# Optimization experiments

Hardware: AMD Instinct MI355X
Metric: run time of the kernel (lower is better)

The kernel has to match this reference:

```python
import jax, jax.numpy as jnp
import numpy as np

B, S, D, H, M = 4, 2048, 1024, 16, 128
DH = D // H
SCALE = jnp.float32(np.sqrt(D / H))


def setup_inputs() -> dict:
    key = jax.random.key(0)
    ks = jax.random.split(key, 4)
    x = jax.random.normal(ks[0], (B, S, D), dtype=jnp.float32)
    mask = jnp.zeros((B, 1, 1, S), dtype=bool)
    W_in = jax.random.normal(ks[1], (3 * D, D), dtype=jnp.float32) * 0.02
    b_in = jnp.zeros((3 * D,), dtype=jnp.float32)
    pos_emb = jax.random.normal(ks[2], (2 * M + 1, DH), dtype=jnp.float32)
    W_out = jax.random.normal(ks[3], (D, D), dtype=jnp.float32) * 0.02
    b_out = jnp.zeros((D,), dtype=jnp.float32)
    return {"x": x, "mask": mask, "W_in": W_in, "b_in": b_in,
            "pos_emb": pos_emb, "W_out": W_out, "b_out": b_out}


def _arrange_pos(pos_emb, seq_len, max_len):
    k = jnp.arange(seq_len)
    q = jnp.arange(seq_len)
    idx = jnp.clip(k[None, :] - q[:, None], -max_len, max_len) + max_len  # [S,S]
    return pos_emb[idx]  # [S,S,DH]


def reference(x, mask, W_in, b_in, pos_emb, W_out, b_out):
    b, s, d = x.shape
    qkv = x @ W_in.T + b_in                      # [B,S,3D]
    qkv = qkv.reshape(b, s, H, 3 * DH).transpose(0, 2, 1, 3)  # [B,H,S,3DH]
    Q, K, V = jnp.split(qkv, 3, axis=3)          # each [B,H,S,DH]
    logits = jnp.einsum('bhqd,bhkd->bhqk', Q, K)
    rel = _arrange_pos(pos_emb, s, M)            # [S,S,DH] (q,k,dh)
    pos_logits = jnp.einsum('bhqd,qkd->bhqk', Q, rel)
    logits = (logits + pos_logits) / SCALE
    logits = jnp.where(mask, -jnp.inf, logits)
    attn = jax.nn.softmax(logits, axis=3)
    combined = jnp.einsum('bhqk,bhkd->bhqd', attn, V)
    out = combined.transpose(0, 2, 1, 3).reshape(b, s, d)  # concat heads
    return out @ W_out.T + b_out
```

## Files before the change

### kernel.cpp

```cpp
#include <hip/hip_runtime.h>
#include <hip/hip_bf16.h>
#include <math.h>

#define SS 2048
#define HH 16
#define NPOS 257
#define C_SCALE 0.18033688f
#define P_THR 256.0f

typedef short  s16x8 __attribute__((ext_vector_type(8)));
typedef float  f32x4 __attribute__((ext_vector_type(4)));
typedef unsigned u32x4 __attribute__((ext_vector_type(4)));

__device__ __forceinline__ unsigned short f2bf(float f) {
    unsigned u = __builtin_bit_cast(unsigned, f);
    u += 0x7fff + ((u >> 16) & 1);
    return (unsigned short)(u >> 16);
}
__device__ __forceinline__ float bf2f(unsigned short b) {
    return __builtin_bit_cast(float, (unsigned)b << 16);
}
__device__ __forceinline__ s16x8 pack8(float4 a, float4 b) {
    s16x8 v;
    v[0]=(short)f2bf(a.x); v[1]=(short)f2bf(a.y); v[2]=(short)f2bf(a.z); v[3]=(short)f2bf(a.w);
    v[4]=(short)f2bf(b.x); v[5]=(short)f2bf(b.y); v[6]=(short)f2bf(b.z); v[7]=(short)f2bf(b.w);
    return v;
}
__device__ __forceinline__ unsigned cvtpk(float lo, float hi) {
    unsigned r;
    asm("v_cvt_pk_bf16_f32 %0, %1, %2" : "=v"(r) : "v"(lo), "v"(hi));
    return r;
}
__device__ __forceinline__ float exp2_fast(float x) {
    float r;
    asm("v_exp_f32 %0, %1" : "=v"(r) : "v"(x));
    return r;
}
__device__ __forceinline__ f32x4 mfma16(s16x8 a, s16x8 b, f32x4 c) {
    return __builtin_amdgcn_mfma_f32_16x16x32_bf16(a, b, c, 0, 0, 0);
}
__device__ __forceinline__ void gload_lds16(const void* gsrc, void* ldst) {
    __builtin_amdgcn_global_load_lds(
        (const __attribute__((address_space(1))) unsigned int*)gsrc,
        (__attribute__((address_space(3))) unsigned int*)ldst,
        16, 0, 0);
}
__device__ __forceinline__ int colp(int k) {
    return ((k >> 5) << 6) | (((k >> 2) & 3) << 4) | (((k >> 4) & 1) << 3) | ((k & 3) << 1);
}

__global__ __launch_bounds__(256)
void cvt_bf16(const float* __restrict__ in, unsigned short* __restrict__ out, int n8)
{
    for (int i = blockIdx.x * blockDim.x + threadIdx.x; i < n8; i += gridDim.x * blockDim.x) {
        const float4* p = (const float4*)(in + (size_t)i * 8);
        *(s16x8*)(out + (size_t)i * 8) = pack8(p[0], p[1]);
    }
}

__global__ __launch_bounds__(256)
void gemm_bf16_nt(const unsigned short* __restrict__ A,
                  const unsigned short* __restrict__ Bm,
                  const float* __restrict__ bias, float* __restrict__ Cout,
                  int Ndim, int Kdim)
{
    __shared__ short As[128 * 32];
    __shared__ short Bs[128 * 32];
    const int tid  = threadIdx.x;
    const int lane = tid & 63;
    const int wv   = tid >> 6;
    const int g    = lane >> 4;
    const int ln   = lane & 15;
    const int wm   = wv >> 1, wn = wv & 1;
    const int tm   = blockIdx.y << 7, tn = blockIdx.x << 7;
    const int srow  = lane >> 2;
    const int sslot = lane & 3;

    f32x4 acc[4][4];
#pragma unroll
    for (int mi = 0; mi < 4; ++mi)
#pragma unroll
        for (int ni = 0; ni < 4; ++ni) acc[mi][ni] = f32x4{0.f, 0.f, 0.f, 0.f};

    const unsigned short* Ab = A  + (size_t)(tm + wv*32 + srow) * Kdim + sslot*8;
    const unsigned short* Bb = Bm + (size_t)(tn + wv*32 + srow) * Kdim + sslot*8;
    const size_t rstep16 = (size_t)16 * Kdim;
    char* lA = (char*)As + (wv*32) * 64;
    char* lB = (char*)Bs + (wv*32) * 64;

    for (int k0 = 0; k0 < Kdim; k0 += 32) {
        __syncthreads();
        gload_lds16(Ab + k0,           lA);
        gload_lds16(Ab + k0 + rstep16, lA + 1024);
        gload_lds16(Bb + k0,           lB);
        gload_lds16(Bb + k0 + rstep16, lB + 1024);
        __syncthreads();

        s16x8 af[4], bf_[4];
#pragma unroll
        for (int mi = 0; mi < 4; ++mi)
            af[mi] = *(const s16x8*)((char*)As + (wm*64 + mi*16 + ln)*64 + g*16);
#pragma unroll
        for (int ni = 0; ni < 4; ++ni)
            bf_[ni] = *(const s16x8*)((char*)Bs + (wn*64 + ni*16 + ln)*64 + g*16);
#pragma unroll
        for (int mi = 0; mi < 4; ++mi)
#pragma unroll
            for (int ni = 0; ni < 4; ++ni)
                acc[mi][ni] = mfma16(af[mi], bf_[ni], acc[mi][ni]);
    }

#pragma unroll
    for (int ni = 0; ni < 4; ++ni) {
        const int col = tn + wn*64 + ni*16 + ln;
        const float bcol = bias[col];
#pragma unroll
        for (int mi = 0; mi < 4; ++mi)
#pragma unroll
            for (int j = 0; j < 4; ++j) {
                const int row = tm + wm*64 + mi*16 + 4*g + j;
                Cout[(size_t)row * Ndim + col] = acc[mi][ni][j] + bcol;
            }
    }
}

__global__ __launch_bounds__(256)
void gemm_qkv(const unsigned short* __restrict__ A,
              const unsigned short* __restrict__ Bm,
              const float* __restrict__ bias,
              unsigned short* __restrict__ qb,
              char* __restrict__ kbuf, char* __restrict__ vbuf)
{
    __shared__ short As[128 * 32];
    __shared__ short Bs[128 * 32];
    const int tid  = threadIdx.x;
    const int lane = tid & 63;
    const int wv   = tid >> 6;
    const int g    = lane >> 4;
    const int ln   = lane & 15;
    const int wm   = wv >> 1, wn = wv & 1;
    const int tm   = blockIdx.y << 7, tn = blockIdx.x << 7;
    const int srow  = lane >> 2;
    const int sslot = lane & 3;
    const int Kdim = 1024;

    f32x4 acc[4][4];
#pragma unroll
    for (int mi = 0; mi < 4; ++mi)
#pragma unroll
        for (int ni = 0; ni < 4; ++ni) acc[mi][ni] = f32x4{0.f, 0.f, 0.f, 0.f};

    const unsigned short* Ab = A  + (size_t)(tm + wv*32 + srow) * Kdim + sslot*8;
    const unsigned short* Bb = Bm + (size_t)(tn + wv*32 + srow) * Kdim + sslot*8;
    const size_t rstep16 = (size_t)16 * Kdim;
    char* lA = (char*)As + (wv*32) * 64;
    char* lB = (char*)Bs + (wv*32) * 64;

    for (int k0 = 0; k0 < Kdim; k0 += 32) {
        __syncthreads();
        gload_lds16(Ab + k0,           lA);
        gload_lds16(Ab + k0 + rstep16, lA + 1024);
        gload_lds16(Bb + k0,           lB);
        gload_lds16(Bb + k0 + rstep16, lB + 1024);
        __syncthreads();

        s16x8 af[4], bf_[4];
#pragma unroll
        for (int mi = 0; mi < 4; ++mi)
            af[mi] = *(const s16x8*)((char*)As + (wm*64 + mi*16 + ln)*64 + g*16);
#pragma unroll
        for (int ni = 0; ni < 4; ++ni)
            bf_[ni] = *(const s16x8*)((char*)Bs + (wn*64 + ni*16 + ln)*64 + g*16);
#pragma unroll
        for (int mi = 0; mi < 4; ++mi)
#pragma unroll
            for (int ni = 0; ni < 4; ++ni)
                acc[mi][ni] = mfma16(af[mi], bf_[ni], acc[mi][ni]);
    }

#pragma unroll
    for (int ni = 0; ni < 4; ++ni) {
        const int col  = tn + wn*64 + ni*16 + ln;
        const int col0 = tn + wn*64 + ni*16;
        const int h    = col0 / 192;
        const int r0   = col0 - h*192;
        const int r    = r0 + ln;
        const float bcol = bias[col];
#pragma unroll
        for (int mi = 0; mi < 4; ++mi) {
            const int rowb = tm + wm*64 + mi*16 + 4*g;
            const int bb = rowb >> 11, sl = rowb & 2047;
            const int kt = sl >> 6, kr = sl & 63;
            const size_t tile = ((size_t)(bb*HH + h)*32 + kt) * 8192;
            if (r0 < 64) {
                unsigned short* qp = qb + (((size_t)(bb*HH + h))*SS + sl)*64 + r;
#pragma unroll
                for (int j = 0; j < 4; ++j)
                    qp[(size_t)j*64] = f2bf((acc[mi][ni][j] + bcol) * C_SCALE);
            } else if (r0 < 128) {
                const int d = r - 64;
#pragma unroll
                for (int j = 0; j < 4; ++j) {
                    const int krj = kr + j;
                    *(unsigned short*)(kbuf + tile + krj*128 + ((2*d) ^ ((krj&7)<<4))) =
                        f2bf(acc[mi][ni][j] + bcol);
                }
            } else {
                const int d = r - 128;
                uint2 w;
                w.x = cvtpk(acc[mi][ni][0] + bcol, acc[mi][ni][1] + bcol);
                w.y = cvtpk(acc[mi][ni][2] + bcol, acc[mi][ni][3] + bcol);
                *(uint2*)(vbuf + tile + d*128 + (colp(kr) ^ ((d&7)<<4))) = w;
            }
        }
    }
}

#define FAR_LDS  32768
#define NEAR_LDS (16384 + 64*260*2)

__global__ __launch_bounds__(256, 4)
void attn_far(const unsigned short* __restrict__ qb,
              const char* __restrict__ kbuf, const char* __restrict__ vbuf,
              const unsigned short* __restrict__ pos_bf,
              float* __restrict__ o_state,
              float* __restrict__ m_state,
              float* __restrict__ l_state)
{
    extern __shared__ char smem[];
    char* ksb = smem;
    char* vtb = smem + 16384;

    const int tid = threadIdx.x, lane = tid & 63, wv = tid >> 6;
    const int g = lane >> 4, ln = lane & 15;
    const int fid = ((blockIdx.x & 7) << 7) | (blockIdx.x >> 3);
    const int q0 = (fid & 15) << 7, h = (fid >> 4) & 15, b = fid >> 8;
    const int q0w = q0 + wv*32;
    const int swz = (ln & 7) << 4;

    const unsigned short* qhb = qb + ((size_t)(b*HH + h))*SS*64;
    const char* ktile = kbuf + (size_t)(b*HH + h)*32*8192;
    const char* vtile = vbuf + (size_t)(b*HH + h)*32*8192;

    s16x8 qf[2][2];
#pragma unroll
    for (int gg = 0; gg < 2; ++gg) {
        const unsigned short* qp = qhb + (size_t)(q0w + 16*gg + ln) * 64;
        qf[gg][0] = *(const s16x8*)(qp + 8*g);
        qf[gg][1] = *(const s16x8*)(qp + 32 + 8*g);
    }

    const int ktA = max(0, (q0 - 128) >> 6);
    const int ktB = min(32, (q0 + 256) >> 6);
    const int gap = ktB - ktA, nfar = 32 - gap;

    char* kd0 = ksb + wv*2048;         char* kd1 = kd0 + 8192;
    char* vd0 = vtb + wv*2048;         char* vd1 = vd0 + 8192;
    const char* kbse0 = ksb + ln*128 + ((g*16) ^ swz);
    const char* kbse1 = ksb + ln*128 + ((64 + g*16) ^ swz);
    const char* vbse0 = vtb + ln*128 + ((g*16) ^ swz);
    const char* vbse1 = vtb + ln*128 + ((64 + g*16) ^ swz);

    const int sq0 = (ktA > 0) ? 0 : gap;
    const int sq1 = (1 < ktA) ? 1 : 1 + gap;
    const int sq2 = (2 < ktA) ? 2 : 2 + gap;

    {
        const char* s0k = ktile + (size_t)sq0*8192 + wv*2048 + lane*16;
        const char* s0v = vtile + (size_t)sq0*8192 + wv*2048 + lane*16;
        gload_lds16(s0k, kd0); gload_lds16(s0k + 1024, kd0 + 1024);
        gload_lds16(s0v, vd0); gload_lds16(s0v + 1024, vd0 + 1024);
        const char* s1k = ktile + (size_t)sq1*8192 + wv*2048 + lane*16;
        const char* s1v = vtile + (size_t)sq1*8192 + wv*2048 + lane*16;
        gload_lds16(s1k, kd1); gload_lds16(s1k + 1024, kd1 + 1024);
        gload_lds16(s1v, vd1); gload_lds16(s1v + 1024, vd1 + 1024);
    }
    const char* ksrc = ktile + (size_t)sq2*8192 + wv*2048 + lane*16;
    const char* vsrc = vtile + (size_t)sq2*8192 + wv*2048 + lane*16;

    float blo[2], bhi[2];
    {
        const int bsrc = (ln >> 2) << 4;
        const int s3 = ln & 3;
#pragma unroll
        for (int pass = 0; pass < 2; ++pass) {
            const int c  = pass*256 + ln;
            const int cc = c > 256 ? 256 : c;
            const unsigned short* pp = pos_bf + (size_t)cc * 64;
            s16x8 b0 = *(const s16x8*)(pp + 8*g);
            s16x8 b1 = *(const s16x8*)(pp + 32 + 8*g);
#pragma unroll
            for (int gg = 0; gg < 2; ++gg) {
                f32x4 d = {0,0,0,0};
                d = mfma16(qf[gg][0], b0, d);
                d = mfma16(qf[gg][1], b1, d);
                const float r0 = __shfl(d[0], bsrc, 64);
                const float r1 = __shfl(d[1], bsrc, 64);
                const float r2 = __shfl(d[2], bsrc, 64);
                const float r3 = __shfl(d[3], bsrc, 64);
                const float r = s3 == 0 ? r0 : s3 == 1 ? r1 : s3 == 2 ? r2 : r3;
                if (pass == 0) blo[gg] = r; else bhi[gg] = r;
            }
        }
    }

    f32x4 o[2][4], l[2];
    float m[2];
#pragma unroll
    for (int gg = 0; gg < 2; ++gg) {
        m[gg] = -INFINITY; l[gg] = f32x4{0,0,0,0};
#pragma unroll
        for (int dt = 0; dt < 4; ++dt) o[gg][dt] = f32x4{0,0,0,0};
    }
    s16x8 ONES;
#pragma unroll
    for (int i = 0; i < 8; ++i) ONES[i] = (short)0x3F80;

    asm volatile("s_waitcnt vmcnt(4)" ::: "memory");
    __builtin_amdgcn_sched_barrier(0);
    __builtin_amdgcn_s_barrier();
    __builtin_amdgcn_sched_barrier(0);

#define F_TILE(CUR, vv) do {                                                  \
                                  \
    f32x4 s[2][4];                                                            \
    _Pragma("unroll")                                                         \
    for (int gi = 0; gi < 2; ++gi)                                            \
        _Pragma("unroll")                                                     \
        for (int t = 0; t < 4; ++t) s[gi][t] = f32x4{0,0,0,0};                \
    __builtin_amdgcn_s_setprio(1);                                            \
    _Pragma("unroll")                                                         \
    for (int kc = 0; kc < 2; ++kc) {                                          \
        const char* kbx_ = (kc ? kbse1 : kbse0) + (CUR)*8192;                 \
        s16x8 kf[4];                                                          \
        _Pragma("unroll")                                                     \
        for (int t = 0; t < 4; ++t)                                           \
            kf[t] = *(const s16x8*)(kbx_ + t*2048);                           \
        _Pragma("unroll")                                                     \
        for (int t = 0; t < 4; ++t)                                           \
            _Pragma("unroll")                                                 \
            for (int gi = 0; gi < 2; ++gi)                                    \
                s[gi][t] = mfma16(kf[t], qf[gi][kc], s[gi][t]);               \
    }                                                                         \
    __builtin_amdgcn_s_setprio(0);                                            \
    const bool left_ = (vv) < ktA;                                            \
    u32x4 pa[2][2];                                                           \
    float pmax[2];                                                            \
    _Pragma("unroll")                                                         \
    for (int gi = 0; gi < 2; ++gi) {                                          \
        const float bmv = (left_ ? blo[gi] : bhi[gi]) - m[gi];                \
        float pm = 0.f;                                                       \
        _Pragma("unroll")                                                     \
        for (int t = 0; t < 4; ++t) {                                         \
            const float p0 = exp2_fast(s[gi][t][0] + bmv);                    \
            const float p1 = exp2_fast(s[gi][t][1] + bmv);                    \
            const float p2 = exp2_fast(s[gi][t][2] + bmv);                    \
            const float p3 = exp2_fast(s[gi][t][3] + bmv);                    \
            pm = fmaxf(pm, fmaxf(fmaxf(p0, p1), fmaxf(p2, p3)));              \
            pa[gi][t>>1][2*(t&1)]   = cvtpk(p0, p1);                          \
            pa[gi][t>>1][2*(t&1)+1] = cvtpk(p2, p3);                          \
        }                                                                     \
        pmax[gi] = pm;                                                        \
    }                                                                         \
    if (__any(fmaxf(pmax[0], pmax[1]) > P_THR)) {           \
        _Pragma("unroll")                                                     \
        for (int gi = 0; gi < 2; ++gi) {                                      \
            const float bc = left_ ? blo[gi] : bhi[gi];                       \
            float mr = s[gi][0][0];                                           \
            _Pragma("unroll")                                                 \
            for (int t = 0; t < 4; ++t)                                       \
                _Pragma("unroll")                                             \
                for (int j = 0; j < 4; ++j) mr = fmaxf(mr, s[gi][t][j]);      \
            mr = fmaxf(mr, __shfl_xor(mr, 16, 64));                           \
            mr = fmaxf(mr, __shfl_xor(mr, 32, 64));                           \
            const float nm = fmaxf(m[gi], mr + bc);                           \
            const float corr = exp2_fast(m[gi] - nm);                         \
            m[gi] = nm;                                                       \
            _Pragma("unroll")                                                 \
            for (int j = 0; j < 4; ++j) {                                     \
                const float cj = __shfl(corr, (lane & 48) + 4*g + j, 64);     \
                _Pragma("unroll")                                             \
                for (int dt = 0; dt < 4; ++dt) o[gi][dt][j] *= cj;            \
                l[gi][j] *= cj;                                               \
            }                                                                 \
            const float nb = bc - nm;                                         \
            _Pragma("unroll")                                                 \
            for (int t = 0; t < 4; ++t) {                                     \
                const float p0 = exp2_fast(s[gi][t][0] + nb);                 \
                const float p1 = exp2_fast(s[gi][t][1] + nb);                 \
                const float p2 = exp2_fast(s[gi][t][2] + nb);                 \
                const float p3 = exp2_fast(s[gi][t][3] + nb);                 \
                pa[gi][t>>1][2*(t&1)]   = cvtpk(p0, p1);                      \
                pa[gi][t>>1][2*(t&1)+1] = cvtpk(p2, p3);                      \
            }                                                                 \
        }                                                                     \
    }                                                                         \
    __builtin_amdgcn_s_setprio(1);                                            \
    _Pragma("unroll")                                                         \
    for (int kc = 0; kc < 2; ++kc) {                                          \
        const char* vbx_ = (kc ? vbse1 : vbse0) + (CUR)*8192;                 \
        _Pragma("unroll")                                                     \
        for (int dt = 0; dt < 4; ++dt) {                                      \
            const s16x8 bv = *(const s16x8*)(vbx_ + dt*2048);                 \
            _Pragma("unroll")                                                 \
            for (int gi = 0; gi < 2; ++gi)                                    \
                o[gi][dt] = mfma16(__builtin_bit_cast(s16x8, pa[gi][kc]), bv, o[gi][dt]); \
        }                                                                     \
        _Pragma("unroll")                                                     \
        for (int gi = 0; gi < 2; ++gi)                                        \
            l[gi] = mfma16(__builtin_bit_cast(s16x8, pa[gi][kc]), ONES, l[gi]); \
    }                                                                         \
    __builtin_amdgcn_s_setprio(0);                                            \
                                     \
    __builtin_amdgcn_s_barrier();                                             \
    __builtin_amdgcn_sched_barrier(0);                                        \
                                \
    if ((vv) + 2 < nfar) {                                                    \
        char* dk_ = (CUR) ? kd1 : kd0;                                        \
        char* dv_ = (CUR) ? vd1 : vd0;                                        \
        gload_lds16(ksrc, dk_); gload_lds16(ksrc + 1024, dk_ + 1024);         \
        gload_lds16(vsrc, dv_); gload_lds16(vsrc + 1024, dv_ + 1024);         \
        const int stp_ = (((vv) + 3) == ktA) ? (gap + 1) * 8192 : 8192;       \
        ksrc += stp_; vsrc += stp_;                                           \
    }                                                                         \
     \
    if ((vv) + 1 < nfar) {                                                    \
        if ((vv) + 2 < nfar) { asm volatile("s_waitcnt vmcnt(4)" ::: "memory"); } \
        else                 { asm volatile("s_waitcnt vmcnt(0)" ::: "memory"); } \
        __builtin_amdgcn_sched_barrier(0);                                    \
        __builtin_amdgcn_s_barrier();                                         \
        __builtin_amdgcn_sched_barrier(0);                                    \
    }                                                                         \
} while (0)

    for (int v = 0; v < nfar; v += 2) {
        F_TILE(0, v);
        F_TILE(1, v + 1);
    }

    const size_t rbase = (((size_t)(b*HH + h)) << 11) + q0w;
#pragma unroll
    for (int gg = 0; gg < 2; ++gg) {
        if (lane < 16) m_state[rbase + 16*gg + ln] = m[gg];
        if (ln == 0) {
#pragma unroll
            for (int j = 0; j < 4; ++j) l_state[rbase + 16*gg + 4*g + j] = l[gg][j];
        }
#pragma unroll
        for (int dt = 0; dt < 4; ++dt)
#pragma unroll
            for (int j = 0; j < 4; ++j)
                o_state[(rbase + 16*gg + 4*g + j)*64 + dt*16 + ln] = o[gg][dt][j];
    }
}

__global__ __launch_bounds__(256, 3)
void attn_near(const unsigned short* __restrict__ qb,
               const char* __restrict__ kbuf, const char* __restrict__ vbuf,
               const unsigned short* __restrict__ pos_bf,
               const float* __restrict__ o_state,
               const float* __restrict__ m_state,
               const float* __restrict__ l_state,
               unsigned short* __restrict__ comb)
{
    extern __shared__ char smem[];
    char* ksb = smem;
    unsigned short* tab = (unsigned short*)(smem + 16384);

    const int tid = threadIdx.x, lane = tid & 63, wv = tid >> 6;
    const int g = lane >> 4, ln = lane & 15;
    const int fid = ((blockIdx.x & 7) << 8) | (blockIdx.x >> 3);
    const int q0 = (fid & 31) << 6, h = (fid >> 5) & 15, b = fid >> 9;
    const int q0w = q0 + wv*16;
    const int swz = (ln & 7) << 4;

    const unsigned short* qhb = qb + ((size_t)(b*HH + h))*SS*64;
    const char* ktile = kbuf + (size_t)(b*HH + h)*32*8192;
    const char* vtile = vbuf + (size_t)(b*HH + h)*32*8192;

    s16x8 qf[2];
    {
        const unsigned short* qp = qhb + (size_t)(q0w + ln) * 64;
        qf[0] = *(const s16x8*)(qp + 8*g);
        qf[1] = *(const s16x8*)(qp + 32 + 8*g);
    }

    const int q0p = q0 & ~127;
    const int ktA = max(0, (q0p - 128) >> 6);
    const int ktB = min(32, (q0p + 256) >> 6);
    const int ntile = ktB - ktA;

    const char* ksrcN = ktile + (size_t)(ktA + 1)*8192 + wv*2048 + lane*16;
    char* nkd0 = ksb + wv*2048;        char* nkd1 = nkd0 + 8192;
    const char* kb0 = ksb + ln*128 + ((g*16) ^ swz);
    const char* kb1 = ksb + ln*128 + ((64 + g*16) ^ swz);
    const char* vsr0 = vtile + (size_t)ktA*8192 + ln*128 + ((g*16) ^ swz) + 4096;
    const char* vsr1 = vtile + (size_t)ktA*8192 + ln*128 + ((64 + g*16) ^ swz) + 4096;

    s16x8 vf[8];

    {
        const char* s0 = ktile + (size_t)ktA*8192 + wv*2048 + lane*16;
        gload_lds16(s0, nkd0); gload_lds16(s0 + 1024, nkd0 + 1024);
#pragma unroll
        for (int dt = 0; dt < 4; ++dt) {
            vf[dt]     = *(const s16x8*)(vsr0 + dt*2048 - 4096);
            vf[4 + dt] = *(const s16x8*)(vsr1 + dt*2048 - 4096);
        }
        vsr0 += 8192; vsr1 += 8192;
    }

    for (int ct = 0; ct < 17; ++ct) {
        const int c  = ct*16 + ln;
        const int cc = c > 256 ? 256 : c;
        const unsigned short* pp = pos_bf + (size_t)cc * 64;
        s16x8 b0 = *(const s16x8*)(pp + 8*g);
        s16x8 b1 = *(const s16x8*)(pp + 32 + 8*g);
        f32x4 d = {0,0,0,0};
        d = mfma16(qf[0], b0, d);
        d = mfma16(qf[1], b1, d);
        if (c < NPOS) {
#pragma unroll
            for (int j = 0; j < 4; ++j)
                tab[(16*wv + 4*g + j)*260 + c] = f2bf(d[j]);
        }
    }
    __syncthreads();

    const size_t rbase = (((size_t)(b*HH + h)) << 11) + q0w;
    float m_run = m_state[rbase + ln];
    f32x4 l_acc;
#pragma unroll
    for (int j = 0; j < 4; ++j) l_acc[j] = l_state[rbase + 4*g + j];
    f32x4 o_acc[4];
#pragma unroll
    for (int dt = 0; dt < 4; ++dt)
#pragma unroll
        for (int j = 0; j < 4; ++j)
            o_acc[dt][j] = o_state[(rbase + 4*g + j)*64 + dt*16 + ln];

    const int rowb = (16*wv + ln) * 260;
    const int coff = 4*g - 16*wv - ln + 128 - q0;
    s16x8 ONES;
#pragma unroll
    for (int i = 0; i < 8; ++i) ONES[i] = (short)0x3F80;

#define N_TILE(CUR, vv) do {                                                  \
    if ((vv) + 1 < ntile) {                                                   \
        char* d_ = (CUR) ? nkd0 : nkd1;                                       \
        gload_lds16(ksrcN, d_); gload_lds16(ksrcN + 1024, d_ + 1024);         \
        ksrcN += 8192;                                                        \
    }                                                                         \
    f32x4 s[4];                                                               \
    _Pragma("unroll")                                                         \
    for (int t = 0; t < 4; ++t) s[t] = f32x4{0,0,0,0};                        \
    __builtin_amdgcn_s_setprio(1);                                            \
    _Pragma("unroll")                                                         \
    for (int kc = 0; kc < 2; ++kc) {                                          \
        const char* kbx_ = kc ? kb1 : kb0;                                    \
        s16x8 kf[4];                                                          \
        _Pragma("unroll")                                                     \
        for (int t = 0; t < 4; ++t)                                           \
            kf[t] = *(const s16x8*)(kbx_ + (CUR)*8192 + t*2048);              \
        _Pragma("unroll")                                                     \
        for (int t = 0; t < 4; ++t)                                           \
            s[t] = mfma16(kf[t], qf[kc], s[t]);                               \
    }                                                                         \
    __builtin_amdgcn_s_setprio(0);                                            \
    const int colb = ((ktA + (vv)) << 6) + coff;                              \
    _Pragma("unroll")                                                         \
    for (int t = 0; t < 4; ++t)                                               \
        _Pragma("unroll")                                                     \
        for (int j = 0; j < 4; ++j) {                                         \
            int c = colb + 16*t + j;                                          \
            c = c < 0 ? 0 : (c > 256 ? 256 : c);                              \
            s[t][j] = s[t][j] + bf2f(tab[rowb + c]);                          \
        }                                                                     \
    u32x4 pa[2];                                                              \
    float pm = 0.f;                                                           \
    _Pragma("unroll")                                                         \
    for (int t = 0; t < 4; ++t) {                                             \
        const float p0 = exp2_fast(s[t][0] - m_run);                          \
        const float p1 = exp2_fast(s[t][1] - m_run);                          \
        const float p2 = exp2_fast(s[t][2] - m_run);                          \
        const float p3 = exp2_fast(s[t][3] - m_run);                          \
        pm = fmaxf(pm, fmaxf(fmaxf(p0, p1), fmaxf(p2, p3)));                  \
        pa[t>>1][2*(t&1)]   = cvtpk(p0, p1);                                  \
        pa[t>>1][2*(t&1)+1] = cvtpk(p2, p3);                                  \
    }                                                                         \
    if (__any(pm > P_THR)) {                                                  \
        float mr = s[0][0];                                                   \
        _Pragma("unroll")                                                     \
        for (int t = 0; t < 4; ++t)                                           \
            _Pragma("unroll")                                                 \
            for (int j = 0; j < 4; ++j) mr = fmaxf(mr, s[t][j]);              \
        mr = fmaxf(mr, __shfl_xor(mr, 16, 64));                               \
        mr = fmaxf(mr, __shfl_xor(mr, 32, 64));                               \
        const float nm = fmaxf(m_run, mr);                                    \
        const float corr = exp2_fast(m_run - nm);                             \
        m_run = nm;                                                           \
        _Pragma("unroll")                                                     \
        for (int j = 0; j < 4; ++j) {                                         \
            const float cj = __shfl(corr, (lane & 48) + 4*g + j, 64);         \
            _Pragma("unroll")                                                 \
            for (int dt = 0; dt < 4; ++dt) o_acc[dt][j] *= cj;                \
            l_acc[j] *= cj;                                                   \
        }                                                                     \
        _Pragma("unroll")                                                     \
        for (int t = 0; t < 4; ++t) {                                         \
            const float p0 = exp2_fast(s[t][0] - m_run);                      \
            const float p1 = exp2_fast(s[t][1] - m_run);                      \
            const float p2 = exp2_fast(s[t][2] - m_run);                      \
            const float p3 = exp2_fast(s[t][3] - m_run);                      \
            pa[t>>1][2*(t&1)]   = cvtpk(p0, p1);                              \
            pa[t>>1][2*(t&1)+1] = cvtpk(p2, p3);                              \
        }                                                                     \
    }                                                                         \
    __builtin_amdgcn_s_setprio(1);                                            \
    _Pragma("unroll")                                                         \
    for (int kc = 0; kc < 2; ++kc) {                                          \
        const s16x8 pA_ = __builtin_bit_cast(s16x8, pa[kc]);                  \
        _Pragma("unroll")                                                     \
        for (int dt = 0; dt < 4; ++dt)                                        \
            o_acc[dt] = mfma16(pA_, vf[kc*4 + dt], o_acc[dt]);                \
        l_acc = mfma16(pA_, ONES, l_acc);                                     \
    }                                                                         \
    __builtin_amdgcn_s_setprio(0);                                            \
    if ((vv) + 1 < ntile) {                                                   \
        _Pragma("unroll")                                                     \
        for (int dt = 0; dt < 4; ++dt) {                                      \
            vf[dt]     = *(const s16x8*)(vsr0 + dt*2048 - 4096);              \
            vf[4 + dt] = *(const s16x8*)(vsr1 + dt*2048 - 4096);              \
        }                                                                     \
        vsr0 += 8192; vsr1 += 8192;                                           \
    }                                                                         \
    __syncthreads();                                                          \
} while (0)

    for (int v = 0; v < ntile; v += 2) {
        N_TILE(0, v);
        N_TILE(1, v + 1);
    }

    f32x4 inv;
#pragma unroll
    for (int j = 0; j < 4; ++j) inv[j] = 1.0f / l_acc[j];
#pragma unroll
    for (int dt = 0; dt < 4; ++dt)
#pragma unroll
        for (int j = 0; j < 4; ++j)
            comb[((size_t)b*SS + q0w + 4*g + j)*1024 + h*64 + dt*16 + ln] =
                f2bf(o_acc[dt][j] * inv[j]);
}

extern "C" void kernel_launch(void* const* d_in, const int* in_sizes, int n_in,
                              void* d_out, int out_size, void* d_ws, size_t ws_size,
                              hipStream_t stream)
{
    const float* x     = (const float*)d_in[0];
    const float* W_in  = (const float*)d_in[2];
    const float* b_in  = (const float*)d_in[3];
    const float* pos   = (const float*)d_in[4];
    const float* W_out = (const float*)d_in[5];
    const float* b_out = (const float*)d_in[6];
    float* out = (float*)d_out;

    char* ws = (char*)d_ws;
    unsigned short* q_buf   = (unsigned short*)(ws);
    char*           k_buf   = (char*)          (ws +  16777216);
    char*           v_buf   = (char*)          (ws +  33554432);
    unsigned short* comb_bf = (unsigned short*)(ws +  50331648);
    unsigned short* x_bf    = (unsigned short*)(ws +  67108864);
    unsigned short* wi_bf   = (unsigned short*)(ws +  83886080);
    unsigned short* wo_bf   = (unsigned short*)(ws +  90177536);
    unsigned short* pos_bf  = (unsigned short*)(ws +  92274688);
    float*          o_state = (float*)        (ws +  92340224);
    float*          m_state = (float*)        (ws + 125894656);
    float*          l_state = (float*)        (ws + 126418944);

    cvt_bf16<<<2048, 256, 0, stream>>>(x,     x_bf,  8192*1024/8);
    cvt_bf16<<<1024, 256, 0, stream>>>(W_in,  wi_bf, 3072*1024/8);
    cvt_bf16<<<512,  256, 0, stream>>>(W_out, wo_bf, 1024*1024/8);
    cvt_bf16<<<9,    256, 0, stream>>>(pos,   pos_bf, 2056);

    gemm_qkv<<<dim3(24, 64), 256, 0, stream>>>(x_bf, wi_bf, b_in, q_buf, k_buf, v_buf);

    (void)hipFuncSetAttribute((const void*)attn_far,
                              hipFuncAttributeMaxDynamicSharedMemorySize, FAR_LDS);
    attn_far<<<dim3(1024), 256, FAR_LDS, stream>>>(q_buf, k_buf, v_buf, pos_bf,
                                                   o_state, m_state, l_state);

    (void)hipFuncSetAttribute((const void*)attn_near,
                              hipFuncAttributeMaxDynamicSharedMemorySize, NEAR_LDS);
    attn_near<<<dim3(2048), 256, NEAR_LDS, stream>>>(q_buf, k_buf, v_buf, pos_bf,
                                                     o_state, m_state, l_state, comb_bf);

    gemm_bf16_nt<<<dim3(8, 64), 256, 0, stream>>>(comb_bf, wo_bf, b_out, out, 1024, 1024);
}
```

Before: 250.5 us.

## Double far-attention query tile to 256 rows per block for K/V reuse

The far-region attention kernel now handles 256 query rows per block (64 per wave, four 16-row groups) instead of 128, halving the grid and the K/V tile loads per query. Score computation is split into two half-passes so the register footprint stays bounded, and the near/far boundary is widened to match the coarser block alignment, which shifts more tiles to the near kernel. The cost is lower occupancy (launch bounds 4→2), only 512 blocks in the grid, and more near-kernel work.

```diff
diff --git a/kernel.cpp b/kernel.cpp
--- a/kernel.cpp
+++ b/kernel.cpp
@@ -219,7 +219,7 @@
 #define FAR_LDS  32768
 #define NEAR_LDS (16384 + 64*260*2)
 
-__global__ __launch_bounds__(256, 4)
+__global__ __launch_bounds__(256, 2)
 void attn_far(const unsigned short* __restrict__ qb,
               const char* __restrict__ kbuf, const char* __restrict__ vbuf,
               const unsigned short* __restrict__ pos_bf,
@@ -233,25 +233,25 @@
 
     const int tid = threadIdx.x, lane = tid & 63, wv = tid >> 6;
     const int g = lane >> 4, ln = lane & 15;
-    const int fid = ((blockIdx.x & 7) << 7) | (blockIdx.x >> 3);
-    const int q0 = (fid & 15) << 7, h = (fid >> 4) & 15, b = fid >> 8;
-    const int q0w = q0 + wv*32;
+    const int fid = ((blockIdx.x & 7) << 6) | (blockIdx.x >> 3);
+    const int q0 = (fid & 7) << 8, h = (fid >> 3) & 15, b = fid >> 7;
+    const int q0w = q0 + wv*64;
     const int swz = (ln & 7) << 4;
 
     const unsigned short* qhb = qb + ((size_t)(b*HH + h))*SS*64;
     const char* ktile = kbuf + (size_t)(b*HH + h)*32*8192;
     const char* vtile = vbuf + (size_t)(b*HH + h)*32*8192;
 
-    s16x8 qf[2][2];
-#pragma unroll
-    for (int gg = 0; gg < 2; ++gg) {
+    s16x8 qf[4][2];
+#pragma unroll
+    for (int gg = 0; gg < 4; ++gg) {
         const unsigned short* qp = qhb + (size_t)(q0w + 16*gg + ln) * 64;
         qf[gg][0] = *(const s16x8*)(qp + 8*g);
         qf[gg][1] = *(const s16x8*)(qp + 32 + 8*g);
     }
 
     const int ktA = max(0, (q0 - 128) >> 6);
-    const int ktB = min(32, (q0 + 256) >> 6);
+    const int ktB = min(32, (q0 + 384) >> 6);
     const int gap = ktB - ktA, nfar = 32 - gap;
 
     char* kd0 = ksb + wv*2048;         char* kd1 = kd0 + 8192;
@@ -278,7 +278,7 @@
     const char* ksrc = ktile + (size_t)sq2*8192 + wv*2048 + lane*16;
     const char* vsrc = vtile + (size_t)sq2*8192 + wv*2048 + lane*16;
 
-    float blo[2], bhi[2];
+    float blo[4], bhi[4];
     {
         const int bsrc = (ln >> 2) << 4;
         const int s3 = ln & 3;
@@ -290,7 +290,7 @@
             s16x8 b0 = *(const s16x8*)(pp + 8*g);
             s16x8 b1 = *(const s16x8*)(pp + 32 + 8*g);
 #pragma unroll
-            for (int gg = 0; gg < 2; ++gg) {
+            for (int gg = 0; gg < 4; ++gg) {
                 f32x4 d = {0,0,0,0};
                 d = mfma16(qf[gg][0], b0, d);
                 d = mfma16(qf[gg][1], b1, d);
@@ -304,10 +304,10 @@
         }
     }
 
-    f32x4 o[2][4], l[2];
-    float m[2];
-#pragma unroll
-    for (int gg = 0; gg < 2; ++gg) {
+    f32x4 o[4][4], l[4];
+    float m[4];
+#pragma unroll
+    for (int gg = 0; gg < 4; ++gg) {
         m[gg] = -INFINITY; l[gg] = f32x4{0,0,0,0};
 #pragma unroll
         for (int dt = 0; dt < 4; ++dt) o[gg][dt] = f32x4{0,0,0,0};
@@ -322,79 +322,85 @@
     __builtin_amdgcn_sched_barrier(0);
 
 #define F_TILE(CUR, vv) do {                                                  \
-                                  \
-    f32x4 s[2][4];                                                            \
+    const bool left_ = (vv) < ktA;                                            \
+    u32x4 pa[4][2];                                                           \
+                       \
     _Pragma("unroll")                                                         \
-    for (int gi = 0; gi < 2; ++gi)                                            \
-        _Pragma("unroll")                                                     \
-        for (int t = 0; t < 4; ++t) s[gi][t] = f32x4{0,0,0,0};                \
-    __builtin_amdgcn_s_setprio(1);                                            \
-    _Pragma("unroll")                                                         \
-    for (int kc = 0; kc < 2; ++kc) {                                          \
-        const char* kbx_ = (kc ? kbse1 : kbse0) + (CUR)*8192;                 \
-        s16x8 kf[4];                                                          \
-        _Pragma("unroll")                                                     \
-        for (int t = 0; t < 4; ++t)                                           \
-            kf[t] = *(const s16x8*)(kbx_ + t*2048);                           \
-        _Pragma("unroll")                                                     \
-        for (int t = 0; t < 4; ++t)                                           \
+    for (int hf = 0; hf < 2; ++hf) {                                          \
+        f32x4 s[2][4];                                                        \
+        _Pragma("unroll")                                                     \
+        for (int gi = 0; gi < 2; ++gi)                                        \
             _Pragma("unroll")                                                 \
-            for (int gi = 0; gi < 2; ++gi)                                    \
-                s[gi][t] = mfma16(kf[t], qf[gi][kc], s[gi][t]);               \
-    }                                                                         \
-    __builtin_amdgcn_s_setprio(0);                                            \
-    const bool left_ = (vv) < ktA;                                            \
-    u32x4 pa[2][2];                                                           \
-    float pmax[2];                                                            \
-    _Pragma("unroll")                                                         \
-    for (int gi = 0; gi < 2; ++gi) {                                          \
-        const float bmv = (left_ ? blo[gi] : bhi[gi]) - m[gi];                \
-        float pm = 0.f;                                                       \
-        _Pragma("unroll")                                                     \
-        for (int t = 0; t < 4; ++t) {                                         \
-            const float p0 = exp2_fast(s[gi][t][0] + bmv);                    \
-            const float p1 = exp2_fast(s[gi][t][1] + bmv);                    \
-            const float p2 = exp2_fast(s[gi][t][2] + bmv);                    \
-            const float p3 = exp2_fast(s[gi][t][3] + bmv);                    \
-            pm = fmaxf(pm, fmaxf(fmaxf(p0, p1), fmaxf(p2, p3)));              \
-            pa[gi][t>>1][2*(t&1)]   = cvtpk(p0, p1);                          \
-            pa[gi][t>>1][2*(t&1)+1] = cvtpk(p2, p3);                          \
-        }                                                                     \
-        pmax[gi] = pm;                                                        \
-    }                                                                         \
-    if (__any(fmaxf(pmax[0], pmax[1]) > P_THR)) {           \
-        _Pragma("unroll")                                                     \
-        for (int gi = 0; gi < 2; ++gi) {                                      \
-            const float bc = left_ ? blo[gi] : bhi[gi];                       \
-            float mr = s[gi][0][0];                                           \
+            for (int t = 0; t < 4; ++t) s[gi][t] = f32x4{0,0,0,0};            \
+        __builtin_amdgcn_s_setprio(1);                                        \
+        _Pragma("unroll")                                                     \
+        for (int kc = 0; kc < 2; ++kc) {                                      \
+            const char* kbx_ = (kc ? kbse1 : kbse0) + (CUR)*8192;             \
+            s16x8 kf[4];                                                      \
+            _Pragma("unroll")                                                 \
+            for (int t = 0; t < 4; ++t)                                       \
+                kf[t] = *(const s16x8*)(kbx_ + t*2048);                       \
             _Pragma("unroll")                                                 \
             for (int t = 0; t < 4; ++t)                                       \
                 _Pragma("unroll")                                             \
-                for (int j = 0; j < 4; ++j) mr = fmaxf(mr, s[gi][t][j]);      \
-            mr = fmaxf(mr, __shfl_xor(mr, 16, 64));                           \
-            mr = fmaxf(mr, __shfl_xor(mr, 32, 64));                           \
-            const float nm = fmaxf(m[gi], mr + bc);                           \
-            const float corr = exp2_fast(m[gi] - nm);                         \
-            m[gi] = nm;                                                       \
-            _Pragma("unroll")                                                 \
-            for (int j = 0; j < 4; ++j) {                                     \
-                const float cj = __shfl(corr, (lane & 48) + 4*g + j, 64);     \
-                _Pragma("unroll")                                             \
-                for (int dt = 0; dt < 4; ++dt) o[gi][dt][j] *= cj;            \
-                l[gi][j] *= cj;                                               \
-            }                                                                 \
-            const float nb = bc - nm;                                         \
+                for (int gi = 0; gi < 2; ++gi)                                \
+                    s[gi][t] = mfma16(kf[t], qf[2*hf + gi][kc], s[gi][t]);    \
+        }                                                                     \
+        __builtin_amdgcn_s_setprio(0);                                        \
+        float pmax[2];                                                        \
+        _Pragma("unroll")                                                     \
+        for (int gi = 0; gi < 2; ++gi) {                                      \
+            const int gg = 2*hf + gi;                                         \
+            const float bmv = (left_ ? blo[gg] : bhi[gg]) - m[gg];            \
+            float pm = 0.f;                                                   \
             _Pragma("unroll")                                                 \
             for (int t = 0; t < 4; ++t) {                                     \
-                const float p0 = exp2_fast(s[gi][t][0] + nb);                 \
-                const float p1 = exp2_fast(s[gi][t][1] + nb);                 \
-                const float p2 = exp2_fast(s[gi][t][2] + nb);                 \
-                const float p3 = exp2_fast(s[gi][t][3] + nb);                 \
-                pa[gi][t>>1][2*(t&1)]   = cvtpk(p0, p1);                      \
-                pa[gi][t>>1][2*(t&1)+1] = cvtpk(p2, p3);                      \
+                const float p0 = exp2_fast(s[gi][t][0] + bmv);                \
+                const float p1 = exp2_fast(s[gi][t][1] + bmv);                \
+                const float p2 = exp2_fast(s[gi][t][2] + bmv);                \
+                const float p3 = exp2_fast(s[gi][t][3] + bmv);                \
+                pm = fmaxf(pm, fmaxf(fmaxf(p0, p1), fmaxf(p2, p3)));          \
+                pa[gg][t>>1][2*(t&1)]   = cvtpk(p0, p1);                      \
+                pa[gg][t>>1][2*(t&1)+1] = cvtpk(p2, p3);                      \
+            }                                                                 \
+            pmax[gi] = pm;                                                    \
+        }                                                                     \
+        if (__any(fmaxf(pmax[0], pmax[1]) > P_THR)) {       \
+            _Pragma("unroll")                                                 \
+            for (int gi = 0; gi < 2; ++gi) {                                  \
+                const int gg = 2*hf + gi;                                     \
+                const float bc = left_ ? blo[gg] : bhi[gg];                   \
+                float mr = s[gi][0][0];                                       \
+                _Pragma("unroll")                                             \
+                for (int t = 0; t < 4; ++t)                                   \
+                    _Pragma("unroll")                                         \
+                    for (int j = 0; j < 4; ++j) mr = fmaxf(mr, s[gi][t][j]);  \
+                mr = fmaxf(mr, __shfl_xor(mr, 16, 64));                       \
+                mr = fmaxf(mr, __shfl_xor(mr, 32, 64));                       \
+                const float nm = fmaxf(m[gg], mr + bc);                       \
+                const float corr = exp2_fast(m[gg] - nm);                     \
+                m[gg] = nm;                                                   \
+                _Pragma("unroll")                                             \
+                for (int j = 0; j < 4; ++j) {                                 \
+                    const float cj = __shfl(corr, (lane & 48) + 4*g + j, 64); \
+                    _Pragma("unroll")                                         \
+                    for (int dt = 0; dt < 4; ++dt) o[gg][dt][j] *= cj;        \
+                    l[gg][j] *= cj;                                           \
+                }                                                             \
+                const float nb = bc - nm;                                     \
+                _Pragma("unroll")                                             \
+                for (int t = 0; t < 4; ++t) {                                 \
+                    const float p0 = exp2_fast(s[gi][t][0] + nb);             \
+                    const float p1 = exp2_fast(s[gi][t][1] + nb);             \
+                    const float p2 = exp2_fast(s[gi][t][2] + nb);             \
+                    const float p3 = exp2_fast(s[gi][t][3] + nb);             \
+                    pa[gg][t>>1][2*(t&1)]   = cvtpk(p0, p1);                  \
+                    pa[gg][t>>1][2*(t&1)+1] = cvtpk(p2, p3);                  \
+                }                                                             \
             }                                                                 \
         }                                                                     \
     }                                                                         \
+                \
     __builtin_amdgcn_s_setprio(1);                                            \
     _Pragma("unroll")                                                         \
     for (int kc = 0; kc < 2; ++kc) {                                          \
@@ -403,12 +409,12 @@
         for (int dt = 0; dt < 4; ++dt) {                                      \
             const s16x8 bv = *(const s16x8*)(vbx_ + dt*2048);                 \
             _Pragma("unroll")                                                 \
-            for (int gi = 0; gi < 2; ++gi)                                    \
-                o[gi][dt] = mfma16(__builtin_bit_cast(s16x8, pa[gi][kc]), bv, o[gi][dt]); \
+            for (int gg = 0; gg < 4; ++gg)                                    \
+                o[gg][dt] = mfma16(__builtin_bit_cast(s16x8, pa[gg][kc]), bv, o[gg][dt]); \
         }                                                                     \
         _Pragma("unroll")                                                     \
-        for (int gi = 0; gi < 2; ++gi)                                        \
-            l[gi] = mfma16(__builtin_bit_cast(s16x8, pa[gi][kc]), ONES, l[gi]); \
+        for (int gg = 0; gg < 4; ++gg)                                        \
+            l[gg] = mfma16(__builtin_bit_cast(s16x8, pa[gg][kc]), ONES, l[gg]); \
     }                                                                         \
     __builtin_amdgcn_s_setprio(0);                                            \
                                      \
@@ -440,7 +446,7 @@
 
     const size_t rbase = (((size_t)(b*HH + h)) << 11) + q0w;
 #pragma unroll
-    for (int gg = 0; gg < 2; ++gg) {
+    for (int gg = 0; gg < 4; ++gg) {
         if (lane < 16) m_state[rbase + 16*gg + ln] = m[gg];
         if (ln == 0) {
 #pragma unroll
@@ -485,9 +491,9 @@
         qf[1] = *(const s16x8*)(qp + 32 + 8*g);
     }
 
-    const int q0p = q0 & ~127;
+    const int q0p = q0 & ~255;
     const int ktA = max(0, (q0p - 128) >> 6);
-    const int ktB = min(32, (q0p + 256) >> 6);
+    const int ktB = min(32, (q0p + 384) >> 6);
     const int ntile = ktB - ktA;
 
     const char* ksrcN = ktile + (size_t)(ktA + 1)*8192 + wv*2048 + lane*16;
@@ -687,8 +693,8 @@
 
     (void)hipFuncSetAttribute((const void*)attn_far,
                               hipFuncAttributeMaxDynamicSharedMemorySize, FAR_LDS);
-    attn_far<<<dim3(1024), 256, FAR_LDS, stream>>>(q_buf, k_buf, v_buf, pos_bf,
-                                                   o_state, m_state, l_state);
+    attn_far<<<dim3(512), 256, FAR_LDS, stream>>>(q_buf, k_buf, v_buf, pos_bf,
+                                                  o_state, m_state, l_state);
 
     (void)hipFuncSetAttribute((const void*)attn_near,
                               hipFuncAttributeMaxDynamicSharedMemorySize, NEAR_LDS);
```

Result: no change. 254.0 us (+1.4%).
